# Performance work log

Measured on AMD Instinct MI355X. Metric: run time of the kernel, lower is better.

## Reference

```python
import jax, jax.numpy as jnp
from jax import lax
import numpy as np


def setup_inputs() -> dict:
    key = jax.random.key(0)
    ks = jax.random.split(key, 5)
    T, B, I, H = 512, 64, 1024, 1024
    s_ih = 1.0 / np.sqrt(I)
    s_hh = 1.0 / np.sqrt(H)
    return {
        "x": jax.random.normal(ks[0], (T, B, I), dtype=jnp.float32),
        "W_ih": jax.random.normal(ks[1], (4 * H, I), dtype=jnp.float32) * s_ih,
        "W_hh": jax.random.normal(ks[2], (4 * H, H), dtype=jnp.float32) * s_hh,
        "b_ih": jax.random.normal(ks[3], (4 * H,), dtype=jnp.float32) * s_ih,
        "b_hh": jax.random.normal(ks[4], (4 * H,), dtype=jnp.float32) * s_hh,
    }


def reference(x, W_ih, W_hh, b_ih, b_hh):
    # x: [T, B, I]; W_ih: [4H, I]; W_hh: [4H, H]; gate order i, f, g, o (torch LSTMCell)
    T, B, _ = x.shape
    H = W_hh.shape[1]
    # Precompute input contributions for all timesteps in one big GEMM.
    xg = jnp.einsum("tbi,gi->tbg", x, W_ih) + b_ih + b_hh  # [T, B, 4H]
    Whh_T = W_hh.T  # [H, 4H]

    def step(carry, xg_t):
        h, c = carry
        gates = xg_t + h @ Whh_T  # [B, 4H]
        i, f, g, o = jnp.split(gates, 4, axis=-1)
        i = jax.nn.sigmoid(i)
        f = jax.nn.sigmoid(f)
        g = jnp.tanh(g)
        o = jax.nn.sigmoid(o)
        c_new = f * c + i * g
        h_new = o * jnp.tanh(c_new)
        return (h_new, c_new), None

    h0 = jnp.zeros((B, H), dtype=x.dtype)
    c0 = jnp.zeros((B, H), dtype=x.dtype)
    (h, c), _ = lax.scan(step, (h0, c0), xg)
    return h  # [B, H] — final hidden state, matching the torch module
```

## Files before the change

kernel.cpp:

```cpp
#include <hip/hip_runtime.h>


#define TT 512
#define BB 64
#define II 1024
#define HHH 1024
#define G4 4096
#define NBLK 128
#define HPB 8

typedef __attribute__((ext_vector_type(8))) short short8;
typedef __attribute__((ext_vector_type(4))) float f32x4;
typedef __attribute__((ext_vector_type(4))) int i32x4;

typedef __attribute__((address_space(1))) const void gvoid;
typedef __attribute__((address_space(3))) void lvoid;

__device__ __forceinline__ short8 load_frag(const unsigned short* p) {
  i32x4 v = *(const i32x4*)p;
  return __builtin_bit_cast(short8, v);
}

__device__ __forceinline__ unsigned short f2bf(float f) {
  unsigned u = __builtin_bit_cast(unsigned, f);
  u = (u + 0x7FFFu + ((u >> 16) & 1u)) >> 16;
  return (unsigned short)u;
}

__device__ __forceinline__ float sigm(float x) {
  return 1.0f / (1.0f + __expf(-x));
}
__device__ __forceinline__ float tanh_f(float x) {
  return 2.0f / (1.0f + __expf(-2.0f * x)) - 1.0f;
}

__global__ void cvt_bf16(const float* __restrict__ s,
                         unsigned short* __restrict__ d, int n4) {
  int stride = gridDim.x * blockDim.x;
  for (int i = blockIdx.x * blockDim.x + threadIdx.x; i < n4; i += stride) {
    f32x4 v = *(const f32x4*)(s + 4 * i);
    unsigned lo = (unsigned)f2bf(v[0]) | ((unsigned)f2bf(v[1]) << 16);
    unsigned hi = (unsigned)f2bf(v[2]) | ((unsigned)f2bf(v[3]) << 16);
    uint2 u; u.x = lo; u.y = hi;
    *(uint2*)(d + 4 * i) = u;
  }
}

__global__ void bias_sum(const float* __restrict__ a,
                         const float* __restrict__ b,
                         float* __restrict__ o) {
  int i = blockIdx.x * blockDim.x + threadIdx.x;
  if (i < G4) o[i] = a[i] + b[i];
}

__global__ __launch_bounds__(256, 1) void xg_gemm(
    const unsigned short* __restrict__ xb,
    const unsigned short* __restrict__ wih,
    const float* __restrict__ bsum,
    char* __restrict__ xg, int xg32)
{
  const int tid = threadIdx.x;
  const int wid = tid >> 6;
  const int lane = tid & 63;
  const int ln15 = lane & 15;
  const int quad = lane >> 4;
  const int bid = blockIdx.x;
  const int cb = (bid & 7) | ((bid >> 4) << 3);
  const int t0 = ((bid >> 3) & 1) * 256;
  const int hc0 = cb * HPB;
  const int koff = wid * 256;

  __shared__ float red[4][64][36];
  __shared__ __align__(16) short xstage[4][2][4096];

  short8 bfrag[8][2];
#pragma unroll
  for (int nt = 0; nt < 2; ++nt) {
    int n = nt * 16 + ln15;
    int grow = (n >> 3) * 1024 + hc0 + (n & 7);
#pragma unroll
    for (int kc = 0; kc < 8; ++kc) {
      int k = koff + kc * 32 + quad * 8;
      bfrag[kc][nt] = load_frag(wih + grow * 1024 + k);
    }
  }

  const int eb = tid >> 2;
  const int erp = tid & 3;
  float bsv[4][2];
#pragma unroll
  for (int q = 0; q < 4; ++q)
#pragma unroll
    for (int rr = 0; rr < 2; ++rr)
      bsv[q][rr] = bsum[q * 1024 + hc0 + erp * 2 + rr];

  const unsigned xrow = (unsigned)(lane >> 3);
  const unsigned xlane = xrow * 2048u + (unsigned)wid * 512u +
                         (((unsigned)(lane & 7) ^ xrow) * 16u);
  const unsigned lsw = (unsigned)(ln15 & 7) << 4;
  const unsigned q16 = (unsigned)quad * 16u;

  f32x4 acc[4][2];

  auto stage_x = [&](int t, int ck, int buf) {
    short* lb = &xstage[wid][buf][0];
    const char* gt = (const char*)xb + (size_t)t * 131072u;
#pragma unroll
    for (int j = 0; j < 8; ++j) {
      unsigned off = xlane + (unsigned)j * 16384u + (unsigned)ck * 128u;
      __builtin_amdgcn_global_load_lds((gvoid*)(gt + off),
                                       (lvoid*)(lb + j * 512), 16, 0, 0);
    }
  };
  auto comp_x = [&](int ck, int buf) {
    const char* lb = (const char*)&xstage[wid][buf][0];
#pragma unroll
    for (int kl = 0; kl < 2; ++kl) {
      int kc = ck * 2 + kl;
#pragma unroll
      for (int m = 0; m < 4; ++m) {
        unsigned loff = (unsigned)m * 2048u + (unsigned)ln15 * 128u +
                        (((unsigned)kl * 64u + q16) ^ lsw);
        short8 a = *(const short8*)(lb + loff);
        acc[m][0] = __builtin_amdgcn_mfma_f32_16x16x32_bf16(
            a, bfrag[kc][0], acc[m][0], 0, 0, 0);
        acc[m][1] = __builtin_amdgcn_mfma_f32_16x16x32_bf16(
            a, bfrag[kc][1], acc[m][1], 0, 0, 0);
      }
    }
  };

  stage_x(t0, 0, 0);
  stage_x(t0, 1, 1);

#pragma unroll 1
  for (int ti = 0; ti < 256; ++ti) {
    const int t = t0 + ti;
#pragma unroll
    for (int m = 0; m < 4; ++m)
#pragma unroll
      for (int nt = 0; nt < 2; ++nt)
        acc[m][nt] = (f32x4){0.0f, 0.0f, 0.0f, 0.0f};

    asm volatile("s_waitcnt vmcnt(8)" ::: "memory");
    comp_x(0, 0);
    asm volatile("s_waitcnt lgkmcnt(0)" ::: "memory");
    stage_x(t, 2, 0);
    asm volatile("s_waitcnt vmcnt(8)" ::: "memory");
    comp_x(1, 1);
    asm volatile("s_waitcnt lgkmcnt(0)" ::: "memory");
    stage_x(t, 3, 1);
    asm volatile("s_waitcnt vmcnt(8)" ::: "memory");
    comp_x(2, 0);
    asm volatile("s_waitcnt vmcnt(0)" ::: "memory");
    comp_x(3, 1);

#pragma unroll
    for (int m = 0; m < 4; ++m)
#pragma unroll
      for (int nt = 0; nt < 2; ++nt)
#pragma unroll
        for (int p = 0; p < 4; ++p)
          red[wid][m * 16 + quad * 4 + p][nt * 16 + ln15] = acc[m][nt][p];

    asm volatile("s_waitcnt lgkmcnt(0)" ::: "memory");
    __builtin_amdgcn_s_barrier();

    size_t xoff = (((size_t)cb * 512 + (size_t)t) * 64 + (size_t)eb) * 32 +
                  (size_t)(erp * 2);
    float s[4][2];
#pragma unroll
    for (int rr = 0; rr < 2; ++rr) {
      int r = erp * 2 + rr;
#pragma unroll
      for (int q = 0; q < 4; ++q) {
        int col = q * 8 + r;
        s[q][rr] = red[0][eb][col] + red[1][eb][col] + red[2][eb][col] +
                   red[3][eb][col] + bsv[q][rr];
      }
    }
    if (xg32) {
      float* xp = (float*)xg + xoff;
#pragma unroll
      for (int q = 0; q < 4; ++q) {
        float2 v; v.x = s[q][0]; v.y = s[q][1];
        *(float2*)(xp + q * 8) = v;
      }
    } else {
      unsigned short* xp = (unsigned short*)xg + xoff;
#pragma unroll
      for (int q = 0; q < 4; ++q) {
        unsigned u = (unsigned)f2bf(s[q][0]) | ((unsigned)f2bf(s[q][1]) << 16);
        *(unsigned*)(xp + q * 8) = u;
      }
    }

    if (ti < 255) {
      stage_x(t + 1, 0, 0);
      stage_x(t + 1, 1, 1);
    }
    asm volatile("s_waitcnt lgkmcnt(0)" ::: "memory");
    __builtin_amdgcn_s_barrier();
  }
}

__global__ __launch_bounds__(256, 1) void lstm_persist(
    const unsigned short* __restrict__ whh,
    const char* __restrict__ xg, int xg32,
    unsigned short* __restrict__ hbuf,
    unsigned int* __restrict__ barrier_mem,
    float* __restrict__ out)
{
  const int tid = threadIdx.x;
  const int wid = tid >> 6;
  const int lane = tid & 63;
  const int ln15 = lane & 15;
  const int quad = lane >> 4;
  const int cb = blockIdx.x;
  const int hc0 = cb * HPB;
  const int koff = wid * 256;

  unsigned int* epoch = barrier_mem;
  unsigned int* root = barrier_mem + 32;
  unsigned int* leaf = barrier_mem + 64 + (cb >> 4) * 32;

  __shared__ float red[4][64][36];
  __shared__ __align__(16) short hstage[4][2][4096];
  __shared__ unsigned ready;

  short8 bfrag[8][2];
#pragma unroll
  for (int nt = 0; nt < 2; ++nt) {
    int n = nt * 16 + ln15;
    int grow = (n >> 3) * 1024 + hc0 + (n & 7);
#pragma unroll
    for (int kc = 0; kc < 8; ++kc) {
      int k = koff + kc * 32 + quad * 8;
      bfrag[kc][nt] = load_frag(whh + grow * 1024 + k);
    }
  }

  const int eb = tid >> 2;
  const int erp = tid & 3;
  const size_t xbase0 = (((size_t)cb * 512) * 64 + (size_t)eb) * 32 +
                        (size_t)(erp * 2);

  if (tid == 0) ready = 0u;
  __syncthreads();

  float cst[2] = {0.0f, 0.0f};
  f32x4 acc[4][2];

  auto stage = [&](const char* gsrc, int ck, int buf) {
    short* lb = &hstage[wid][buf][0];
    const char* gs = gsrc + wid * 32768 + ck * 8192 + (unsigned)lane * 16u;
#pragma unroll
    for (int j = 0; j < 8; ++j) {
      __builtin_amdgcn_global_load_lds((gvoid*)(gs + j * 1024),
                                       (lvoid*)(lb + j * 512),
                                       16, 0, 0x11);
    }
  };
  auto comp = [&](int ck, int buf) {
    const char* lb = (const char*)&hstage[wid][buf][0];
#pragma unroll
    for (int kl = 0; kl < 2; ++kl) {
      int kc = ck * 2 + kl;
#pragma unroll
      for (int m = 0; m < 4; ++m) {
        unsigned loff = (unsigned)(kl * 4 + quad) * 1024u +
                        (unsigned)(m * 16 + ln15) * 16u;
        short8 a = *(const short8*)(lb + loff);
        acc[m][0] = __builtin_amdgcn_mfma_f32_16x16x32_bf16(
            a, bfrag[kc][0], acc[m][0], 0, 0, 0);
        acc[m][1] = __builtin_amdgcn_mfma_f32_16x16x32_bf16(
            a, bfrag[kc][1], acc[m][1], 0, 0, 0);
      }
    }
  };

#pragma unroll 1
  for (int t = 0; t < TT; ++t) {
    float xgv[4][2];
    if (xg32) {
      const float* xp = (const float*)xg + xbase0 + (size_t)t * 2048u;
#pragma unroll
      for (int q = 0; q < 4; ++q) {
        float2 v = *(const float2*)(xp + q * 8);
        xgv[q][0] = v.x; xgv[q][1] = v.y;
      }
    } else {
      const unsigned short* xp =
          (const unsigned short*)xg + xbase0 + (size_t)t * 2048u;
#pragma unroll
      for (int q = 0; q < 4; ++q) {
        unsigned u = *(const unsigned*)(xp + q * 8);
        xgv[q][0] = __builtin_bit_cast(float, u << 16);
        xgv[q][1] = __builtin_bit_cast(float, u & 0xffff0000u);
      }
    }

#pragma unroll
    for (int m = 0; m < 4; ++m)
#pragma unroll
      for (int nt = 0; nt < 2; ++nt)
        acc[m][nt] = (f32x4){0.0f, 0.0f, 0.0f, 0.0f};

    if (t) {
      if (wid == 0) {
        if (lane == 0) {
          while (__hip_atomic_load(epoch, __ATOMIC_RELAXED,
                                   __HIP_MEMORY_SCOPE_AGENT) < (unsigned)t)
            __builtin_amdgcn_s_sleep(1);
          __hip_atomic_store(&ready, (unsigned)t, __ATOMIC_RELAXED,
                             __HIP_MEMORY_SCOPE_WORKGROUP);
        }
      } else {
        while (__hip_atomic_load(&ready, __ATOMIC_RELAXED,
                                 __HIP_MEMORY_SCOPE_WORKGROUP) < (unsigned)t)
          __builtin_amdgcn_s_sleep(1);
      }

      const char* gsrc = (const char*)(hbuf + (t & 1) * 65536);
      stage(gsrc, 0, 0);
      stage(gsrc, 1, 1);
      asm volatile("s_waitcnt vmcnt(8)" ::: "memory");
      comp(0, 0);
      asm volatile("s_waitcnt lgkmcnt(0)" ::: "memory");
      stage(gsrc, 2, 0);
      asm volatile("s_waitcnt vmcnt(8)" ::: "memory");
      comp(1, 1);
      asm volatile("s_waitcnt lgkmcnt(0)" ::: "memory");
      stage(gsrc, 3, 1);
      asm volatile("s_waitcnt vmcnt(8)" ::: "memory");
      comp(2, 0);
      asm volatile("s_waitcnt vmcnt(0)" ::: "memory");
      comp(3, 1);
    }

#pragma unroll
    for (int m = 0; m < 4; ++m)
#pragma unroll
      for (int nt = 0; nt < 2; ++nt)
#pragma unroll
        for (int p = 0; p < 4; ++p)
          red[wid][m * 16 + quad * 4 + p][nt * 16 + ln15] = acc[m][nt][p];

    asm volatile("s_waitcnt lgkmcnt(0)" ::: "memory");
    __builtin_amdgcn_s_barrier();

    float hv[2];
#pragma unroll
    for (int rr = 0; rr < 2; ++rr) {
      int r = erp * 2 + rr;
      float g[4];
#pragma unroll
      for (int q = 0; q < 4; ++q) {
        int col = q * 8 + r;
        g[q] = red[0][eb][col] + red[1][eb][col] + red[2][eb][col] +
               red[3][eb][col] + xgv[q][rr];
      }
      float ig = sigm(g[0]);
      float fg = sigm(g[1]);
      float gg = tanh_f(g[2]);
      float og = sigm(g[3]);
      float c = fg * cst[rr] + ig * gg;
      cst[rr] = c;
      hv[rr] = og * tanh_f(c);
    }
    unsigned hpack = (unsigned)f2bf(hv[0]) | ((unsigned)f2bf(hv[1]) << 16);
    __hip_atomic_store(
        (unsigned*)(hbuf + ((t + 1) & 1) * 65536 + cb * 512 + eb * 8 +
                    erp * 2),
        hpack, __ATOMIC_RELAXED, __HIP_MEMORY_SCOPE_AGENT);

    if (t == TT - 1) {
      float2 o2; o2.x = hv[0]; o2.y = hv[1];
      *(float2*)(out + eb * HHH + hc0 + erp * 2) = o2;
    }

    __syncthreads();

    if (t < TT - 1 && tid == 0) {
      unsigned old = atomicAdd(leaf, 1u);
      if (old == (unsigned)t * 16u + 15u) {
        unsigned old2 = atomicAdd(root, 1u);
        if (old2 == (unsigned)t * 8u + 7u)
          atomicExch(epoch, (unsigned)(t + 1));
      }
    }
  }
}

extern "C" void kernel_launch(void* const* d_in, const int* in_sizes, int n_in,
                              void* d_out, int out_size, void* d_ws,
                              size_t ws_size, hipStream_t stream) {
  (void)in_sizes; (void)n_in; (void)out_size;
  const float* x   = (const float*)d_in[0];
  const float* wih = (const float*)d_in[1];
  const float* whh = (const float*)d_in[2];
  const float* bih = (const float*)d_in[3];
  const float* bhh = (const float*)d_in[4];

  char* ws = (char*)d_ws;
  unsigned int*   bar  = (unsigned int*)(ws);
  unsigned short* hb   = (unsigned short*)(ws + 4096);
  unsigned short* wihb = (unsigned short*)(ws + (1ull << 20));
  unsigned short* whhb = (unsigned short*)(ws + (9ull << 20));
  float*          bs   = (float*)(ws + (17ull << 20));
  unsigned short* xb   = (unsigned short*)(ws + (18ull << 20));
  char*           xg   = ws + (96ull << 20);
  int xg32 = (ws_size >= (640ull << 20)) ? 1 : 0;

  hipMemsetAsync(ws, 0, 4096, stream);

  cvt_bf16<<<2048, 256, 0, stream>>>(x, xb, (TT * BB * II) / 4);
  cvt_bf16<<<1024, 256, 0, stream>>>(wih, wihb, (G4 * II) / 4);
  cvt_bf16<<<1024, 256, 0, stream>>>(whh, whhb, (G4 * HHH) / 4);
  bias_sum<<<16, 256, 0, stream>>>(bih, bhh, bs);

  xg_gemm<<<256, 256, 0, stream>>>(xb, wihb, bs, xg, xg32);
  lstm_persist<<<NBLK, 256, 0, stream>>>(whhb, xg, xg32, hb, bar,
                                         (float*)d_out);
}
```

Measured before the change: 3.483 ms.

## Replace tree barrier with per-block flags and restructure xg GEMM split

The persistent LSTM kernel drops the hierarchical atomic-counter barrier. Each block now publishes its own step flag, and every wave polls all 128 flags with a wave-wide vote, then applies an acquire fence. The xg load moves after the wait, h staging uses triple buffering with deeper prefetch, and the cache-policy bits on the LDS loads are cleared. The input GEMM is re-split so each block handles half the batch for all timesteps, using a rotating three-buffer x stage. The aim is shorter per-step synchronisation latency, at the cost of more polling traffic and possible memory-ordering risk from the relaxed stores.

```diff
diff --git a/kernel.cpp b/kernel.cpp
--- a/kernel.cpp
+++ b/kernel.cpp
@@ -64,14 +64,13 @@
   const int lane = tid & 63;
   const int ln15 = lane & 15;
   const int quad = lane >> 4;
-  const int bid = blockIdx.x;
-  const int cb = (bid & 7) | ((bid >> 4) << 3);
-  const int t0 = ((bid >> 3) & 1) * 256;
+  const int cb = blockIdx.x >> 1;
+  const int mh = blockIdx.x & 1;
   const int hc0 = cb * HPB;
   const int koff = wid * 256;
 
-  __shared__ float red[4][64][36];
-  __shared__ __align__(16) short xstage[4][2][4096];
+  __shared__ float red[4][32][36];
+  __shared__ __align__(16) short xstage[4][3][4096];
 
   short8 bfrag[8][2];
 #pragma unroll
@@ -85,78 +84,67 @@
     }
   }
 
-  const int eb = tid >> 2;
-  const int erp = tid & 3;
-  float bsv[4][2];
-#pragma unroll
-  for (int q = 0; q < 4; ++q)
-#pragma unroll
-    for (int rr = 0; rr < 2; ++rr)
-      bsv[q][rr] = bsum[q * 1024 + hc0 + erp * 2 + rr];
-
-  const unsigned xrow = (unsigned)(lane >> 3);
-  const unsigned xlane = xrow * 2048u + (unsigned)wid * 512u +
-                         (((unsigned)(lane & 7) ^ xrow) * 16u);
-  const unsigned lsw = (unsigned)(ln15 & 7) << 4;
-  const unsigned q16 = (unsigned)quad * 16u;
-
-  f32x4 acc[4][2];
+  const int eb = tid >> 3;
+  const int er = tid & 7;
+  float bsv[4];
+#pragma unroll
+  for (int q = 0; q < 4; ++q) bsv[q] = bsum[q * 1024 + hc0 + er];
+
+  const unsigned xsl = (unsigned)(lane >> 5) * 2048u +
+                       (unsigned)(lane & 31) * 16u;
+  const size_t wbase = (size_t)(mh * 32) * 2048u + (unsigned)wid * 512u;
+
+  f32x4 acc[2][2];
 
   auto stage_x = [&](int t, int ck, int buf) {
     short* lb = &xstage[wid][buf][0];
-    const char* gt = (const char*)xb + (size_t)t * 131072u;
+    const char* gt = (const char*)xb + (size_t)t * 131072u + wbase +
+                     (unsigned)ck * 32768u + xsl;
 #pragma unroll
     for (int j = 0; j < 8; ++j) {
-      unsigned off = xlane + (unsigned)j * 16384u + (unsigned)ck * 128u;
-      __builtin_amdgcn_global_load_lds((gvoid*)(gt + off),
+      __builtin_amdgcn_global_load_lds((gvoid*)(gt + j * 4096),
                                        (lvoid*)(lb + j * 512), 16, 0, 0);
     }
   };
-  auto comp_x = [&](int ck, int buf) {
+  auto comp_x = [&](int m, int buf) {
     const char* lb = (const char*)&xstage[wid][buf][0];
 #pragma unroll
-    for (int kl = 0; kl < 2; ++kl) {
-      int kc = ck * 2 + kl;
-#pragma unroll
-      for (int m = 0; m < 4; ++m) {
-        unsigned loff = (unsigned)m * 2048u + (unsigned)ln15 * 128u +
-                        (((unsigned)kl * 64u + q16) ^ lsw);
-        short8 a = *(const short8*)(lb + loff);
-        acc[m][0] = __builtin_amdgcn_mfma_f32_16x16x32_bf16(
-            a, bfrag[kc][0], acc[m][0], 0, 0, 0);
-        acc[m][1] = __builtin_amdgcn_mfma_f32_16x16x32_bf16(
-            a, bfrag[kc][1], acc[m][1], 0, 0, 0);
-      }
-    }
-  };
-
-  stage_x(t0, 0, 0);
-  stage_x(t0, 1, 1);
+    for (int kc = 0; kc < 8; ++kc) {
+      unsigned loff = (unsigned)ln15 * 512u + (unsigned)kc * 64u +
+                      (unsigned)quad * 16u;
+      short8 a = *(const short8*)(lb + loff);
+      acc[m][0] = __builtin_amdgcn_mfma_f32_16x16x32_bf16(
+          a, bfrag[kc][0], acc[m][0], 0, 0, 0);
+      acc[m][1] = __builtin_amdgcn_mfma_f32_16x16x32_bf16(
+          a, bfrag[kc][1], acc[m][1], 0, 0, 0);
+    }
+  };
+
+  stage_x(0, 0, 0);
+  stage_x(0, 1, 1);
+  int b0 = 0, b1 = 1, b2 = 2;
 
 #pragma unroll 1
-  for (int ti = 0; ti < 256; ++ti) {
-    const int t = t0 + ti;
-#pragma unroll
-    for (int m = 0; m < 4; ++m)
+  for (int t = 0; t < TT; ++t) {
+#pragma unroll
+    for (int m = 0; m < 2; ++m)
 #pragma unroll
       for (int nt = 0; nt < 2; ++nt)
         acc[m][nt] = (f32x4){0.0f, 0.0f, 0.0f, 0.0f};
 
     asm volatile("s_waitcnt vmcnt(8)" ::: "memory");
-    comp_x(0, 0);
+    comp_x(0, b0);
     asm volatile("s_waitcnt lgkmcnt(0)" ::: "memory");
-    stage_x(t, 2, 0);
+    if (t < TT - 1) stage_x(t + 1, 0, b2);
     asm volatile("s_waitcnt vmcnt(8)" ::: "memory");
-    comp_x(1, 1);
+    comp_x(1, b1);
     asm volatile("s_waitcnt lgkmcnt(0)" ::: "memory");
-    stage_x(t, 3, 1);
-    asm volatile("s_waitcnt vmcnt(8)" ::: "memory");
-    comp_x(2, 0);
-    asm volatile("s_waitcnt vmcnt(0)" ::: "memory");
-    comp_x(3, 1);
-
-#pragma unroll
-    for (int m = 0; m < 4; ++m)
+    if (t < TT - 1) stage_x(t + 1, 1, b0);
+    int nb0 = b2, nb1 = b0, nb2 = b1;
+    b0 = nb0; b1 = nb1; b2 = nb2;
+
+#pragma unroll
+    for (int m = 0; m < 2; ++m)
 #pragma unroll
       for (int nt = 0; nt < 2; ++nt)
 #pragma unroll
@@ -166,40 +154,25 @@
     asm volatile("s_waitcnt lgkmcnt(0)" ::: "memory");
     __builtin_amdgcn_s_barrier();
 
-    size_t xoff = (((size_t)cb * 512 + (size_t)t) * 64 + (size_t)eb) * 32 +
-                  (size_t)(erp * 2);
-    float s[4][2];
-#pragma unroll
-    for (int rr = 0; rr < 2; ++rr) {
-      int r = erp * 2 + rr;
-#pragma unroll
-      for (int q = 0; q < 4; ++q) {
-        int col = q * 8 + r;
-        s[q][rr] = red[0][eb][col] + red[1][eb][col] + red[2][eb][col] +
-                   red[3][eb][col] + bsv[q][rr];
-      }
-    }
+    float g[4];
+#pragma unroll
+    for (int q = 0; q < 4; ++q) {
+      int col = q * 8 + er;
+      g[q] = red[0][eb][col] + red[1][eb][col] + red[2][eb][col] +
+             red[3][eb][col] + bsv[q];
+    }
+    size_t xoff = (((size_t)cb * 512 + (size_t)t) * 64 +
+                   (size_t)(mh * 32 + eb)) * 32 + (size_t)er;
     if (xg32) {
       float* xp = (float*)xg + xoff;
 #pragma unroll
-      for (int q = 0; q < 4; ++q) {
-        float2 v; v.x = s[q][0]; v.y = s[q][1];
-        *(float2*)(xp + q * 8) = v;
-      }
+      for (int q = 0; q < 4; ++q) xp[q * 8] = g[q];
     } else {
       unsigned short* xp = (unsigned short*)xg + xoff;
 #pragma unroll
-      for (int q = 0; q < 4; ++q) {
-        unsigned u = (unsigned)f2bf(s[q][0]) | ((unsigned)f2bf(s[q][1]) << 16);
-        *(unsigned*)(xp + q * 8) = u;
-      }
-    }
-
-    if (ti < 255) {
-      stage_x(t + 1, 0, 0);
-      stage_x(t + 1, 1, 1);
-    }
-    asm volatile("s_waitcnt lgkmcnt(0)" ::: "memory");
+      for (int q = 0; q < 4; ++q) xp[q * 8] = f2bf(g[q]);
+    }
+
     __builtin_amdgcn_s_barrier();
   }
 }
@@ -208,7 +181,7 @@
     const unsigned short* __restrict__ whh,
     const char* __restrict__ xg, int xg32,
     unsigned short* __restrict__ hbuf,
-    unsigned int* __restrict__ barrier_mem,
+    unsigned int* __restrict__ flags,
     float* __restrict__ out)
 {
   const int tid = threadIdx.x;
@@ -220,13 +193,8 @@
   const int hc0 = cb * HPB;
   const int koff = wid * 256;
 
-  unsigned int* epoch = barrier_mem;
-  unsigned int* root = barrier_mem + 32;
-  unsigned int* leaf = barrier_mem + 64 + (cb >> 4) * 32;
-
   __shared__ float red[4][64][36];
-  __shared__ __align__(16) short hstage[4][2][4096];
-  __shared__ unsigned ready;
+  __shared__ __align__(16) short hstage[4][3][4096];
 
   short8 bfrag[8][2];
 #pragma unroll
@@ -245,11 +213,29 @@
   const size_t xbase0 = (((size_t)cb * 512) * 64 + (size_t)eb) * 32 +
                         (size_t)(erp * 2);
 
-  if (tid == 0) ready = 0u;
-  __syncthreads();
-
   float cst[2] = {0.0f, 0.0f};
   f32x4 acc[4][2];
+  float xgv[4][2];
+
+  auto load_xg = [&](int t) {
+    if (xg32) {
+      const float* xp = (const float*)xg + xbase0 + (size_t)t * 2048u;
+#pragma unroll
+      for (int q = 0; q < 4; ++q) {
+        float2 v = *(const float2*)(xp + q * 8);
+        xgv[q][0] = v.x; xgv[q][1] = v.y;
+      }
+    } else {
+      const unsigned short* xp =
+          (const unsigned short*)xg + xbase0 + (size_t)t * 2048u;
+#pragma unroll
+      for (int q = 0; q < 4; ++q) {
+        unsigned u = *(const unsigned*)(xp + q * 8);
+        xgv[q][0] = __builtin_bit_cast(float, u << 16);
+        xgv[q][1] = __builtin_bit_cast(float, u & 0xffff0000u);
+      }
+    }
+  };
 
   auto stage = [&](const char* gsrc, int ck, int buf) {
     short* lb = &hstage[wid][buf][0];
@@ -258,7 +244,7 @@
     for (int j = 0; j < 8; ++j) {
       __builtin_amdgcn_global_load_lds((gvoid*)(gs + j * 1024),
                                        (lvoid*)(lb + j * 512),
-                                       16, 0, 0x11);
+                                       16, 0, 0);
     }
   };
   auto comp = [&](int ck, int buf) {
@@ -281,25 +267,6 @@
 
 #pragma unroll 1
   for (int t = 0; t < TT; ++t) {
-    float xgv[4][2];
-    if (xg32) {
-      const float* xp = (const float*)xg + xbase0 + (size_t)t * 2048u;
-#pragma unroll
-      for (int q = 0; q < 4; ++q) {
-        float2 v = *(const float2*)(xp + q * 8);
-        xgv[q][0] = v.x; xgv[q][1] = v.y;
-      }
-    } else {
-      const unsigned short* xp =
-          (const unsigned short*)xg + xbase0 + (size_t)t * 2048u;
-#pragma unroll
-      for (int q = 0; q < 4; ++q) {
-        unsigned u = *(const unsigned*)(xp + q * 8);
-        xgv[q][0] = __builtin_bit_cast(float, u << 16);
-        xgv[q][1] = __builtin_bit_cast(float, u & 0xffff0000u);
-      }
-    }
-
 #pragma unroll
     for (int m = 0; m < 4; ++m)
 #pragma unroll
@@ -307,35 +274,34 @@
         acc[m][nt] = (f32x4){0.0f, 0.0f, 0.0f, 0.0f};
 
     if (t) {
-      if (wid == 0) {
-        if (lane == 0) {
-          while (__hip_atomic_load(epoch, __ATOMIC_RELAXED,
-                                   __HIP_MEMORY_SCOPE_AGENT) < (unsigned)t)
-            __builtin_amdgcn_s_sleep(1);
-          __hip_atomic_store(&ready, (unsigned)t, __ATOMIC_RELAXED,
-                             __HIP_MEMORY_SCOPE_WORKGROUP);
-        }
-      } else {
-        while (__hip_atomic_load(&ready, __ATOMIC_RELAXED,
-                                 __HIP_MEMORY_SCOPE_WORKGROUP) < (unsigned)t)
-          __builtin_amdgcn_s_sleep(1);
-      }
+      for (;;) {
+        unsigned f0 = __hip_atomic_load(flags + lane, __ATOMIC_RELAXED,
+                                        __HIP_MEMORY_SCOPE_AGENT);
+        unsigned f1 = __hip_atomic_load(flags + 64 + lane, __ATOMIC_RELAXED,
+                                        __HIP_MEMORY_SCOPE_AGENT);
+        if (__all((f0 >= (unsigned)t) && (f1 >= (unsigned)t))) break;
+        __builtin_amdgcn_s_sleep(1);
+      }
+      __builtin_amdgcn_fence(__ATOMIC_ACQUIRE, "agent");
+
+      load_xg(t);
 
       const char* gsrc = (const char*)(hbuf + (t & 1) * 65536);
       stage(gsrc, 0, 0);
       stage(gsrc, 1, 1);
-      asm volatile("s_waitcnt vmcnt(8)" ::: "memory");
+      stage(gsrc, 2, 2);
+      asm volatile("s_waitcnt vmcnt(16)" ::: "memory");
       comp(0, 0);
       asm volatile("s_waitcnt lgkmcnt(0)" ::: "memory");
-      stage(gsrc, 2, 0);
+      stage(gsrc, 3, 0);
+      asm volatile("s_waitcnt vmcnt(16)" ::: "memory");
+      comp(1, 1);
       asm volatile("s_waitcnt vmcnt(8)" ::: "memory");
-      comp(1, 1);
-      asm volatile("s_waitcnt lgkmcnt(0)" ::: "memory");
-      stage(gsrc, 3, 1);
-      asm volatile("s_waitcnt vmcnt(8)" ::: "memory");
-      comp(2, 0);
+      comp(2, 2);
       asm volatile("s_waitcnt vmcnt(0)" ::: "memory");
-      comp(3, 1);
+      comp(3, 0);
+    } else {
+      load_xg(t);
     }
 
 #pragma unroll
@@ -381,14 +347,9 @@
 
     __syncthreads();
 
-    if (t < TT - 1 && tid == 0) {
-      unsigned old = atomicAdd(leaf, 1u);
-      if (old == (unsigned)t * 16u + 15u) {
-        unsigned old2 = atomicAdd(root, 1u);
-        if (old2 == (unsigned)t * 8u + 7u)
-          atomicExch(epoch, (unsigned)(t + 1));
-      }
-    }
+    if (t < TT - 1 && tid == 0)
+      __hip_atomic_store(flags + cb, (unsigned)(t + 1), __ATOMIC_RELAXED,
+                         __HIP_MEMORY_SCOPE_AGENT);
   }
 }
 
@@ -403,7 +364,7 @@
   const float* bhh = (const float*)d_in[4];
 
   char* ws = (char*)d_ws;
-  unsigned int*   bar  = (unsigned int*)(ws);
+  unsigned int*   flg  = (unsigned int*)(ws);
   unsigned short* hb   = (unsigned short*)(ws + 4096);
   unsigned short* wihb = (unsigned short*)(ws + (1ull << 20));
   unsigned short* whhb = (unsigned short*)(ws + (9ull << 20));
@@ -420,6 +381,6 @@
   bias_sum<<<16, 256, 0, stream>>>(bih, bhh, bs);
 
   xg_gemm<<<256, 256, 0, stream>>>(xb, wihb, bs, xg, xg32);
-  lstm_persist<<<NBLK, 256, 0, stream>>>(whhb, xg, xg32, hb, bar,
+  lstm_persist<<<NBLK, 256, 0, stream>>>(whhb, xg, xg32, hb, flg,
                                          (float*)d_out);
 }
```

Measured after the change: 6.250 ms. 79.5% more time.
